# Kernel optimization log

Measured on AMD Instinct MI355X. Metric: run time of the kernel, lower is better.

Reference implementation:

```python
import jax, jax.numpy as jnp
import numpy as np

HEADS = 16
HEAD_DIM = 64
HIDDEN = HEADS * HEAD_DIM  # 1024
COMPRESSION = 1.0  # concat([o, p], -1) forces compressed seq len == T, i.e. scale 1
LN_EPS = 1e-5


def _interp_linear_seq(x, scale):
    # F.interpolate(mode='linear', align_corners=False) along the sequence axis.
    # x: [B, T, C] -> [B, int(T*scale), C]
    T = x.shape[1]
    S = int(T * scale)
    src = (jnp.arange(S, dtype=jnp.float32) + 0.5) / scale - 0.5
    src = jnp.clip(src, 0.0, T - 1)
    lo = jnp.floor(src).astype(jnp.int32)
    hi = jnp.minimum(lo + 1, T - 1)
    w = (src - lo.astype(jnp.float32))[None, :, None]
    return x[:, lo] * (1.0 - w) + x[:, hi] * w


def _rotary(x):
    # rotate-half rotary embedding; x: [B, S, h, d]
    S, d = x.shape[1], x.shape[3]
    inv_freq = 1.0 / (10000.0 ** (jnp.arange(0, d, 2, dtype=jnp.float32) / d))
    ang = jnp.arange(S, dtype=jnp.float32)[:, None] * inv_freq  # [S, d/2]
    cos = jnp.cos(ang)[None, :, None, :]
    sin = jnp.sin(ang)[None, :, None, :]
    x1, x2 = jnp.split(x, 2, axis=-1)
    return jnp.concatenate([x1 * cos - x2 * sin, x1 * sin + x2 * cos], axis=-1)


def setup_inputs() -> dict:
    key = jax.random.key(0)
    ks = jax.random.split(key, 4)
    B, T = 4, 2048
    x = jax.random.normal(ks[0], (B, T, HIDDEN), dtype=jnp.float32)
    ln_gamma = jnp.ones((HIDDEN,), dtype=jnp.float32)
    ln_beta = jnp.zeros((HIDDEN,), dtype=jnp.float32)
    w_in = jax.random.normal(ks[1], (HIDDEN, 7 * HIDDEN), dtype=jnp.float32) * (HIDDEN ** -0.5)
    w_out = jax.random.normal(ks[2], (5 * HIDDEN, HIDDEN), dtype=jnp.float32) * ((5 * HIDDEN) ** -0.5)
    b_out = jnp.zeros((HIDDEN,), dtype=jnp.float32)
    return {"x": x, "ln_gamma": ln_gamma, "ln_beta": ln_beta,
            "w_in": w_in, "w_out": w_out, "b_out": b_out}


def reference(x, ln_gamma, ln_beta, w_in, w_out, b_out):
    B, T, _ = x.shape
    # LayerNorm
    mu = jnp.mean(x, axis=-1, keepdims=True)
    var = jnp.mean(jnp.square(x - mu), axis=-1, keepdims=True)
    xn = (x - mu) / jnp.sqrt(var + LN_EPS) * ln_gamma + ln_beta
    # fused QKVP projection (no bias)
    qkvp = xn @ w_in  # [B, T, 7*HIDDEN]
    q, k, v, p = jnp.split(qkvp, [HIDDEN, 2 * HIDDEN, 3 * HIDDEN], axis=-1)
    # linear-interpolation compression of k, v, p along the sequence axis
    k = _interp_linear_seq(k, COMPRESSION)
    v = _interp_linear_seq(v, COMPRESSION)
    p = _interp_linear_seq(p, COMPRESSION)
    S = k.shape[1]
    q = q.reshape(B, T, HEADS, HEAD_DIM)
    k = k.reshape(B, S, HEADS, HEAD_DIM)
    v = v.reshape(B, S, HEADS, HEAD_DIM)
    q = _rotary(q)
    k = _rotary(k)
    # manual softmax attention (no mask in the original)
    a = jnp.einsum('bihd,bjhd->bhij', q, k) * (HEAD_DIM ** -0.5)
    a = jax.nn.softmax(a, axis=-1)
    o = jnp.einsum('bhij,bjhd->bihd', a, v).reshape(B, T, HIDDEN)
    # GELU side branch (torch F.gelu default = exact erf gelu)
    p = jax.nn.gelu(p, approximate=False)
    return jnp.concatenate([o, p], axis=-1) @ w_out + b_out
```

## Files before the change

### kernel.cpp

```cpp
#include <hip/hip_runtime.h>
#include <hip/hip_bf16.h>
#include <math.h>

typedef short bf16x8 __attribute__((ext_vector_type(8)));
typedef float f32x4 __attribute__((ext_vector_type(4)));
typedef float f32x16 __attribute__((ext_vector_type(16)));

#define HEADS 16
#define HDIM 64
#define HID 1024
#define B_ 4
#define T_ 2048
#define BT_ (B_*T_)
#define N1 (7*HID)
#define K2 (5*HID)

#define SM_SCALE_LOG2E 0.18033688011111793f

__device__ __forceinline__ float bf2f(unsigned short u) {
  union { unsigned int i; float f; } c; c.i = ((unsigned int)u) << 16; return c.f;
}
__device__ __forceinline__ unsigned short f2bf(float f) {
  __hip_bfloat16 h = __float2bfloat16(f);
  return __builtin_bit_cast(unsigned short, h);
}
__device__ __forceinline__ unsigned int cvt_pk_bf16(float a, float b) {
  unsigned int r;
  asm("v_cvt_pk_bf16_f32 %0, %1, %2" : "=v"(r) : "v"(a), "v"(b));
  return r;
}
__device__ __forceinline__ void permswap(unsigned int& d, unsigned int& s) {
  asm volatile("v_permlane32_swap_b32 %0, %1" : "+v"(d), "+v"(s));
}
__device__ __forceinline__ float gelu_fast(float x) {
  float y = 0.7978845608028654f * (x + 0.044715f * x * x * x);
  float e = exp2f(y * 2.8853900817779268f);
  float t = 1.f - 2.f / (e + 1.f);
  return 0.5f * x * (1.f + t);
}

__global__ __launch_bounds__(256) void tcast_kernel(const float* __restrict__ in,
                                                    unsigned short* __restrict__ out,
                                                    int R, int C) {
  __shared__ float tile[64][65];
  int tx = threadIdx.x & 63;
  int ty = threadIdx.x >> 6;
  long r0 = (long)blockIdx.y * 64;
  long c0 = (long)blockIdx.x * 64;
#pragma unroll
  for (int i = 0; i < 16; i++) {
    int r = ty + i * 4;
    tile[r][tx] = in[(r0 + r) * C + c0 + tx];
  }
  __syncthreads();
#pragma unroll
  for (int i = 0; i < 16; i++) {
    int rr = ty + i * 4;
    out[(c0 + rr) * R + r0 + tx] = f2bf(tile[tx][rr]);
  }
}

__global__ __launch_bounds__(256) void ln_kernel(const float* __restrict__ x,
                                                 const float* __restrict__ g,
                                                 const float* __restrict__ b,
                                                 unsigned short* __restrict__ xn) {
  int row = blockIdx.x, tid = threadIdx.x;
  float4 v = reinterpret_cast<const float4*>(x + (long)row * HID)[tid];
  float s = v.x + v.y + v.z + v.w;
  float sq = v.x * v.x + v.y * v.y + v.z * v.z + v.w * v.w;
#pragma unroll
  for (int off = 32; off > 0; off >>= 1) { s += __shfl_down(s, off); sq += __shfl_down(sq, off); }
  __shared__ float red[8];
  int wid = tid >> 6, lane = tid & 63;
  if (lane == 0) { red[wid] = s; red[4 + wid] = sq; }
  __syncthreads();
  if (tid == 0) {
    red[0] = red[0] + red[1] + red[2] + red[3];
    red[4] = red[4] + red[5] + red[6] + red[7];
  }
  __syncthreads();
  float mean = red[0] * (1.f / HID);
  float var  = red[4] * (1.f / HID) - mean * mean;
  float rstd = rsqrtf(var + 1e-5f);
  float4 gv = reinterpret_cast<const float4*>(g)[tid];
  float4 bv = reinterpret_cast<const float4*>(b)[tid];
  ushort4 o;
  o.x = f2bf((v.x - mean) * rstd * gv.x + bv.x);
  o.y = f2bf((v.y - mean) * rstd * gv.y + bv.y);
  o.z = f2bf((v.z - mean) * rstd * gv.z + bv.z);
  o.w = f2bf((v.w - mean) * rstd * gv.w + bv.w);
  reinterpret_cast<ushort4*>(xn + (long)row * HID)[tid] = o;
}

__device__ __forceinline__ void gemm_core_db(const unsigned short* __restrict__ A,
                                             const unsigned short* __restrict__ BT,
                                             unsigned short* As, unsigned short* Bs,
                                             int K, int lda, int ldb,
                                             long row0, long col0,
                                             int lane, int wid, f32x4 (&acc)[4][4]) {
  int l15 = lane & 15, lq = lane >> 4;
  int srow = lane >> 2;
  int schnk = lane & 3;
  int r0s = wid * 32 + srow;
  int r1s = r0s + 16;
  int slot0 = schnk ^ ((r0s >> 1) & 3);
  int slot1 = schnk ^ ((r1s >> 1) & 3);
  const unsigned short* a0 = A + (row0 + r0s) * (long)lda + schnk * 8;
  const unsigned short* a1 = A + (row0 + r1s) * (long)lda + schnk * 8;
  const unsigned short* b0 = BT + (col0 + r0s) * (long)ldb + schnk * 8;
  const unsigned short* b1 = BT + (col0 + r1s) * (long)ldb + schnk * 8;
  int wm = (wid & 1) * 64, wn = (wid >> 1) * 64;
  int NT = K / 32;

  bf16x8 ar0 = *reinterpret_cast<const bf16x8*>(a0);
  bf16x8 ar1 = *reinterpret_cast<const bf16x8*>(a1);
  bf16x8 br0 = *reinterpret_cast<const bf16x8*>(b0);
  bf16x8 br1 = *reinterpret_cast<const bf16x8*>(b1);
  *reinterpret_cast<bf16x8*>(&As[r0s * 32 + slot0 * 8]) = ar0;
  *reinterpret_cast<bf16x8*>(&As[r1s * 32 + slot1 * 8]) = ar1;
  *reinterpret_cast<bf16x8*>(&Bs[r0s * 32 + slot0 * 8]) = br0;
  *reinterpret_cast<bf16x8*>(&Bs[r1s * 32 + slot1 * 8]) = br1;
  ar0 = *reinterpret_cast<const bf16x8*>(a0 + 32);
  ar1 = *reinterpret_cast<const bf16x8*>(a1 + 32);
  br0 = *reinterpret_cast<const bf16x8*>(b0 + 32);
  br1 = *reinterpret_cast<const bf16x8*>(b1 + 32);
  __syncthreads();

  int cur = 0;
  for (int t = 0; t < NT; t++) {
    const unsigned short* Asr = As + cur * 4096;
    const unsigned short* Bsr = Bs + cur * 4096;
    bf16x8 af[4], bfv[4];
#pragma unroll
    for (int m = 0; m < 4; m++) {
      int r = wm + m * 16 + l15;
      af[m] = *reinterpret_cast<const bf16x8*>(&Asr[r * 32 + (lq ^ ((r >> 1) & 3)) * 8]);
    }
#pragma unroll
    for (int n = 0; n < 4; n++) {
      int r = wn + n * 16 + l15;
      bfv[n] = *reinterpret_cast<const bf16x8*>(&Bsr[r * 32 + (lq ^ ((r >> 1) & 3)) * 8]);
    }
    if (t + 1 < NT) {
      unsigned short* Asw = As + (cur ^ 1) * 4096;
      unsigned short* Bsw = Bs + (cur ^ 1) * 4096;
      *reinterpret_cast<bf16x8*>(&Asw[r0s * 32 + slot0 * 8]) = ar0;
      *reinterpret_cast<bf16x8*>(&Asw[r1s * 32 + slot1 * 8]) = ar1;
      *reinterpret_cast<bf16x8*>(&Bsw[r0s * 32 + slot0 * 8]) = br0;
      *reinterpret_cast<bf16x8*>(&Bsw[r1s * 32 + slot1 * 8]) = br1;
    }
    if (t + 2 < NT) {
      long ko = (long)(t + 2) * 32;
      ar0 = *reinterpret_cast<const bf16x8*>(a0 + ko);
      ar1 = *reinterpret_cast<const bf16x8*>(a1 + ko);
      br0 = *reinterpret_cast<const bf16x8*>(b0 + ko);
      br1 = *reinterpret_cast<const bf16x8*>(b1 + ko);
    }
#pragma unroll
    for (int m = 0; m < 4; m++)
#pragma unroll
      for (int n = 0; n < 4; n++)
        acc[m][n] = __builtin_amdgcn_mfma_f32_16x16x32_bf16(af[m], bfv[n], acc[m][n], 0, 0, 0);
    __syncthreads();
    cur ^= 1;
  }
}

__global__ __launch_bounds__(256) void gemm1_fused(const unsigned short* __restrict__ A,
                                                   const unsigned short* __restrict__ BT,
                                                   unsigned short* __restrict__ q_r,
                                                   unsigned short* __restrict__ k_r,
                                                   unsigned short* __restrict__ v_t,
                                                   unsigned short* __restrict__ C5) {
  __shared__ unsigned short smem[18432];
  unsigned short* As = smem;
  unsigned short* Bs = smem + 8192;
  int tid = threadIdx.x, lane = tid & 63, wid = tid >> 6;
  long row0 = (long)blockIdx.y * 128;
  long col0 = (long)blockIdx.x * 128;
  f32x4 acc[4][4] = {};
  gemm_core_db(A, BT, As, Bs, HID, HID, HID, row0, col0, lane, wid, acc);

  int wm = (wid & 1) * 64, wn = (wid >> 1) * 64;
  long row_base = row0 + wm;
  int b = (int)(row_base >> 11);
  int t_base = (int)(row_base & 2047);
  int col_base = (int)col0 + wn;
  int region = col_base >> 10;
  int l15 = lane & 15, lq = lane >> 4;

  if (region <= 1) {
    unsigned short* dst = (region == 0) ? q_r : k_r;
    float osc = (region == 0) ? SM_SCALE_LOG2E : 1.0f;
    int head = (col_base & 1023) >> 6;
    long obase = (long)(b * 16 + head) * T_ * 64;
    float fr[2];
    fr[0] = __expf(-(float)l15 * 0.28782313662425572f);
    fr[1] = __expf(-(float)(16 + l15) * 0.28782313662425572f);
#pragma unroll
    for (int m = 0; m < 4; m++) {
#pragma unroll
      for (int j = 0; j < 4; j++) {
        int t = t_base + m * 16 + lq * 4 + j;
#pragma unroll
        for (int n = 0; n < 2; n++) {
          float sn, cs;
          __sincosf((float)t * fr[n], &sn, &cs);
          float xl = acc[m][n][j], xh = acc[m][n + 2][j];
          int d = n * 16 + l15;
          dst[obase + (long)t * 64 + d]      = f2bf((xl * cs - xh * sn) * osc);
          dst[obase + (long)t * 64 + d + 32] = f2bf((xl * sn + xh * cs) * osc);
        }
      }
    }
  } else if (region == 2) {
    int head = (col_base & 1023) >> 6;
    unsigned short* vt = smem + wid * 4608;
#pragma unroll
    for (int m = 0; m < 4; m++)
#pragma unroll
      for (int n = 0; n < 4; n++)
#pragma unroll
        for (int j = 0; j < 4; j++)
          vt[(n * 16 + l15) * 72 + m * 16 + lq * 4 + j] = f2bf(acc[m][n][j]);
    long obase = (long)(b * 16 + head) * 64 * T_;
#pragma unroll
    for (int i = 0; i < 8; i++) {
      int d = i * 8 + (lane >> 3);
      int tl = (lane & 7) * 8;
      bf16x8 v = *reinterpret_cast<const bf16x8*>(&vt[d * 72 + tl]);
      *reinterpret_cast<bf16x8*>(v_t + obase + (long)d * T_ + t_base + tl) = v;
    }
  } else {
    int colp = col_base - 3 * HID;
#pragma unroll
    for (int m = 0; m < 4; m++) {
#pragma unroll
      for (int j = 0; j < 4; j++) {
        long row = row_base + m * 16 + lq * 4 + j;
#pragma unroll
        for (int n = 0; n < 4; n++)
          C5[row * K2 + HID + colp + n * 16 + l15] = f2bf(gelu_fast(acc[m][n][j]));
      }
    }
  }
}

__global__ __launch_bounds__(256) void gemm_bt(const unsigned short* __restrict__ A,
                                               const unsigned short* __restrict__ BT,
                                               float* __restrict__ Cout,
                                               const float* __restrict__ bias,
                                               int K, int lda, int ldb, int ldc) {
  __shared__ unsigned short smem2[16384];
  unsigned short* As = smem2;
  unsigned short* Bs = smem2 + 8192;
  int tid = threadIdx.x, lane = tid & 63, wid = tid >> 6;
  long row0 = (long)blockIdx.y * 128;
  long col0 = (long)blockIdx.x * 128;
  f32x4 acc[4][4] = {};
  gemm_core_db(A, BT, As, Bs, K, lda, ldb, row0, col0, lane, wid, acc);
  int wm = (wid & 1) * 64, wn = (wid >> 1) * 64;
#pragma unroll
  for (int m = 0; m < 4; m++) {
#pragma unroll
    for (int n = 0; n < 4; n++) {
      long r = row0 + wm + m * 16 + (lane >> 4) * 4;
      long c = col0 + wn + n * 16 + (lane & 15);
#pragma unroll
      for (int j = 0; j < 4; j++)
        Cout[(r + j) * (long)ldc + c] = acc[m][n][j] + bias[c];
    }
  }
}

__global__ __launch_bounds__(256) void attn_kernel(const unsigned short* __restrict__ q_r,
                                                   const unsigned short* __restrict__ k_r,
                                                   const unsigned short* __restrict__ v_t,
                                                   unsigned short* __restrict__ C5) {
  int bh = blockIdx.x;
  int qt = blockIdx.y;
  int b = bh >> 4, h = bh & 15;
  int tid = threadIdx.x, lane = tid & 63, wid = tid >> 6;
  int l31 = lane & 31, hi = lane >> 5;
  __shared__ unsigned short Ks[2][64 * 64];
  __shared__ unsigned short Vts[2][64 * 64];

  const unsigned short* qbase = q_r + ((long)bh * T_ + qt * 128 + wid * 32) * 64;
  bf16x8 qf[4];
#pragma unroll
  for (int kk = 0; kk < 4; kk++)
    qf[kk] = *reinterpret_cast<const bf16x8*>(qbase + l31 * 64 + kk * 16 + hi * 8);

  f32x16 o_acc[2] = {};
  float l_run = 0.f;

  const unsigned short* kbase = k_r + (long)bh * T_ * 64;
  const unsigned short* vbase = v_t + (long)bh * 64 * T_;
  int srow = lane >> 3;
  int schnk = lane & 7;
  int slot = schnk ^ srow;

  bf16x8 kreg[2], vreg[2];
#pragma unroll
  for (int i = 0; i < 2; i++) {
    int c = wid * 2 + i;
    kreg[i] = *reinterpret_cast<const bf16x8*>(kbase + c * 512 + lane * 8);
    vreg[i] = *reinterpret_cast<const bf16x8*>(vbase + (long)(c * 8 + srow) * T_ + schnk * 8);
  }
#pragma unroll
  for (int i = 0; i < 2; i++) {
    int r = (wid * 2 + i) * 8 + srow;
    *reinterpret_cast<bf16x8*>(&Ks[0][r * 64 + slot * 8])  = kreg[i];
    *reinterpret_cast<bf16x8*>(&Vts[0][r * 64 + slot * 8]) = vreg[i];
  }
#pragma unroll
  for (int i = 0; i < 2; i++) {
    int c = wid * 2 + i;
    kreg[i] = *reinterpret_cast<const bf16x8*>(kbase + 4096 + c * 512 + lane * 8);
    vreg[i] = *reinterpret_cast<const bf16x8*>(vbase + (long)(c * 8 + srow) * T_ + 64 + schnk * 8);
  }
  __syncthreads();

  int cur = 0;
  for (int kt = 0; kt < 32; kt++) {
    if (kt < 31) {
#pragma unroll
      for (int i = 0; i < 2; i++) {
        int r = (wid * 2 + i) * 8 + srow;
        *reinterpret_cast<bf16x8*>(&Ks[cur ^ 1][r * 64 + slot * 8])  = kreg[i];
        *reinterpret_cast<bf16x8*>(&Vts[cur ^ 1][r * 64 + slot * 8]) = vreg[i];
      }
    }
    if (kt < 30) {
#pragma unroll
      for (int i = 0; i < 2; i++) {
        int c = wid * 2 + i;
        kreg[i] = *reinterpret_cast<const bf16x8*>(kbase + (kt + 2) * 4096 + c * 512 + lane * 8);
        vreg[i] = *reinterpret_cast<const bf16x8*>(vbase + (long)(c * 8 + srow) * T_ + (kt + 2) * 64 + schnk * 8);
      }
    }
    const unsigned short* Kc = Ks[cur];
    const unsigned short* Vc = Vts[cur];

    bf16x8 pa[4];
#pragma unroll
    for (int t2 = 0; t2 < 2; t2++) {
      f32x16 s2 = {};
      int krow = t2 * 32 + l31;
      __builtin_amdgcn_s_setprio(1);
#pragma unroll
      for (int kk = 0; kk < 4; kk++) {
        int c = kk * 2 + hi;
        bf16x8 kf = *reinterpret_cast<const bf16x8*>(&Kc[krow * 64 + (c ^ (krow & 7)) * 8]);
        s2 = __builtin_amdgcn_mfma_f32_32x32x16_bf16(kf, qf[kk], s2, 0, 0, 0);
      }
      __builtin_amdgcn_s_setprio(0);
      float p[16];
#pragma unroll
      for (int r = 0; r < 16; r++) p[r] = exp2f(s2[r]);
#pragma unroll
      for (int r = 0; r < 16; r++) l_run += p[r];
      unsigned int g0 = cvt_pk_bf16(p[0],  p[1]);
      unsigned int g1 = cvt_pk_bf16(p[2],  p[3]);
      unsigned int g2 = cvt_pk_bf16(p[4],  p[5]);
      unsigned int g3 = cvt_pk_bf16(p[6],  p[7]);
      unsigned int g4 = cvt_pk_bf16(p[8],  p[9]);
      unsigned int g5 = cvt_pk_bf16(p[10], p[11]);
      unsigned int g6 = cvt_pk_bf16(p[12], p[13]);
      unsigned int g7 = cvt_pk_bf16(p[14], p[15]);
      permswap(g0, g2);
      permswap(g1, g3);
      permswap(g4, g6);
      permswap(g5, g7);
      uint4 u0; u0.x = g0; u0.y = g1; u0.z = g2; u0.w = g3;
      uint4 u1; u1.x = g4; u1.y = g5; u1.z = g6; u1.w = g7;
      pa[t2 * 2]     = __builtin_bit_cast(bf16x8, u0);
      pa[t2 * 2 + 1] = __builtin_bit_cast(bf16x8, u1);
    }
    __builtin_amdgcn_s_setprio(1);
#pragma unroll
    for (int dt = 0; dt < 2; dt++) {
      int vrow = dt * 32 + l31;
#pragma unroll
      for (int kc = 0; kc < 4; kc++) {
        int c = kc * 2 + hi;
        bf16x8 vf = *reinterpret_cast<const bf16x8*>(&Vc[vrow * 64 + (c ^ (vrow & 7)) * 8]);
        o_acc[dt] = __builtin_amdgcn_mfma_f32_32x32x16_bf16(pa[kc], vf, o_acc[dt], 0, 0, 0);
      }
    }
    __builtin_amdgcn_s_setprio(0);
    __syncthreads();
    cur ^= 1;
  }
  float l = l_run;
  l += __shfl_xor(l, 32);
#pragma unroll
  for (int r = 0; r < 16; r++) {
    int qr = (r & 3) + 8 * (r >> 2) + 4 * hi;
    float inv = 1.0f / __shfl(l, qr);
    int tl = qt * 128 + wid * 32 + qr;
    long row = (long)b * T_ + tl;
#pragma unroll
    for (int dt = 0; dt < 2; dt++) {
      int col = h * 64 + dt * 32 + l31;
      C5[row * K2 + col] = f2bf(o_acc[dt][r] * inv);
    }
  }
}

extern "C" void kernel_launch(void* const* d_in, const int* in_sizes, int n_in,
                              void* d_out, int out_size, void* d_ws, size_t ws_size,
                              hipStream_t stream) {
  const float* x     = (const float*)d_in[0];
  const float* g     = (const float*)d_in[1];
  const float* be    = (const float*)d_in[2];
  const float* w_in  = (const float*)d_in[3];
  const float* w_out = (const float*)d_in[4];
  const float* b_out = (const float*)d_in[5];
  float* out = (float*)d_out;

  char* ws = (char*)d_ws;
  size_t off = 0;
  auto alloc = [&](size_t bytes) {
    void* p = ws + off;
    off += (bytes + 255) & ~(size_t)255;
    return p;
  };
  unsigned short* xn     = (unsigned short*)alloc((size_t)BT_ * HID * 2);
  unsigned short* w_inT  = (unsigned short*)alloc((size_t)N1 * HID * 2);
  unsigned short* w_outT = (unsigned short*)alloc((size_t)HID * K2 * 2);
  unsigned short* q_rb   = (unsigned short*)alloc((size_t)BT_ * HID * 2);
  unsigned short* k_rb   = (unsigned short*)alloc((size_t)BT_ * HID * 2);
  unsigned short* v_tb   = (unsigned short*)alloc((size_t)BT_ * HID * 2);
  unsigned short* C5     = (unsigned short*)alloc((size_t)BT_ * K2 * 2);

  tcast_kernel<<<dim3(N1 / 64, HID / 64), 256, 0, stream>>>(w_in, w_inT, HID, N1);
  tcast_kernel<<<dim3(HID / 64, K2 / 64), 256, 0, stream>>>(w_out, w_outT, K2, HID);
  ln_kernel<<<BT_, 256, 0, stream>>>(x, g, be, xn);
  gemm1_fused<<<dim3(N1 / 128, BT_ / 128), 256, 0, stream>>>(xn, w_inT, q_rb, k_rb, v_tb, C5);
  attn_kernel<<<dim3(64, T_ / 128), 256, 0, stream>>>(q_rb, k_rb, v_tb, C5);
  gemm_bt<<<dim3(HID / 128, BT_ / 128), 256, 0, stream>>>(C5, w_outT, out, b_out,
                                                          K2, K2, K2, HID);
}
```

Baseline: 413.0 us.

## Enlarge QKVP GEMM tile to 256x128 with 8 waves and direct V^T stores

The fused input-projection GEMM now uses 256-row by 128-column tiles with 512 threads (8 waves in a 4x2 arrangement), so each B tile loaded into shared memory is reused across twice as many rows. This cuts global and LDS traffic per output. The V-transpose epilogue drops its shared-memory staging and writes packed 4-element bf16 chunks straight to global memory, giving up some store coalescing. The larger block doubles the LDS footprint and halves the grid, which may lower occupancy.

```diff
diff --git a/kernel.cpp b/kernel.cpp
--- a/kernel.cpp
+++ b/kernel.cpp
@@ -90,6 +90,138 @@
   o.z = f2bf((v.z - mean) * rstd * gv.z + bv.z);
   o.w = f2bf((v.w - mean) * rstd * gv.w + bv.w);
   reinterpret_cast<ushort4*>(xn + (long)row * HID)[tid] = o;
+}
+
+__global__ __launch_bounds__(512) void gemm1_fused(const unsigned short* __restrict__ A,
+                                                   const unsigned short* __restrict__ BT,
+                                                   unsigned short* __restrict__ q_r,
+                                                   unsigned short* __restrict__ k_r,
+                                                   unsigned short* __restrict__ v_t,
+                                                   unsigned short* __restrict__ C5) {
+  __shared__ unsigned short As[2 * 256 * 32];
+  __shared__ unsigned short Bs[2 * 128 * 32];
+  int tid = threadIdx.x, lane = tid & 63, wid = tid >> 6;
+  int l15 = lane & 15, lq = lane >> 4;
+  int wr = wid >> 1, wc = wid & 1;
+  long row0 = (long)blockIdx.y * 256;
+  long col0 = (long)blockIdx.x * 128;
+  f32x4 acc[4][4] = {};
+
+  int sr0 = tid >> 2;
+  int sr1 = sr0 + 128;
+  int sch = tid & 3;
+  int sl0 = sch ^ ((sr0 >> 1) & 3);
+  int sl1 = sch ^ ((sr1 >> 1) & 3);
+  const unsigned short* a0 = A + (row0 + sr0) * (long)HID + sch * 8;
+  const unsigned short* a1 = A + (row0 + sr1) * (long)HID + sch * 8;
+  const unsigned short* b0 = BT + (col0 + sr0) * (long)HID + sch * 8;
+
+  bf16x8 ar0 = *reinterpret_cast<const bf16x8*>(a0);
+  bf16x8 ar1 = *reinterpret_cast<const bf16x8*>(a1);
+  bf16x8 br0 = *reinterpret_cast<const bf16x8*>(b0);
+  *reinterpret_cast<bf16x8*>(&As[sr0 * 32 + sl0 * 8]) = ar0;
+  *reinterpret_cast<bf16x8*>(&As[sr1 * 32 + sl1 * 8]) = ar1;
+  *reinterpret_cast<bf16x8*>(&Bs[sr0 * 32 + sl0 * 8]) = br0;
+  ar0 = *reinterpret_cast<const bf16x8*>(a0 + 32);
+  ar1 = *reinterpret_cast<const bf16x8*>(a1 + 32);
+  br0 = *reinterpret_cast<const bf16x8*>(b0 + 32);
+  __syncthreads();
+
+  const int NT = HID / 32;
+  int cur = 0;
+  for (int t = 0; t < NT; t++) {
+    const unsigned short* Asr = As + cur * 8192;
+    const unsigned short* Bsr = Bs + cur * 4096;
+    bf16x8 af[4], bfv[4];
+#pragma unroll
+    for (int m = 0; m < 4; m++) {
+      int r = wr * 64 + m * 16 + l15;
+      af[m] = *reinterpret_cast<const bf16x8*>(&Asr[r * 32 + (lq ^ ((r >> 1) & 3)) * 8]);
+    }
+#pragma unroll
+    for (int n = 0; n < 4; n++) {
+      int r = wc * 64 + n * 16 + l15;
+      bfv[n] = *reinterpret_cast<const bf16x8*>(&Bsr[r * 32 + (lq ^ ((r >> 1) & 3)) * 8]);
+    }
+    if (t + 1 < NT) {
+      unsigned short* Asw = As + (cur ^ 1) * 8192;
+      unsigned short* Bsw = Bs + (cur ^ 1) * 4096;
+      *reinterpret_cast<bf16x8*>(&Asw[sr0 * 32 + sl0 * 8]) = ar0;
+      *reinterpret_cast<bf16x8*>(&Asw[sr1 * 32 + sl1 * 8]) = ar1;
+      *reinterpret_cast<bf16x8*>(&Bsw[sr0 * 32 + sl0 * 8]) = br0;
+    }
+    if (t + 2 < NT) {
+      long ko = (long)(t + 2) * 32;
+      ar0 = *reinterpret_cast<const bf16x8*>(a0 + ko);
+      ar1 = *reinterpret_cast<const bf16x8*>(a1 + ko);
+      br0 = *reinterpret_cast<const bf16x8*>(b0 + ko);
+    }
+#pragma unroll
+    for (int m = 0; m < 4; m++)
+#pragma unroll
+      for (int n = 0; n < 4; n++)
+        acc[m][n] = __builtin_amdgcn_mfma_f32_16x16x32_bf16(af[m], bfv[n], acc[m][n], 0, 0, 0);
+    __syncthreads();
+    cur ^= 1;
+  }
+
+  long row_base = row0 + wr * 64;
+  int b = (int)(row_base >> 11);
+  int t_base = (int)(row_base & 2047);
+  int col_base = (int)col0 + wc * 64;
+  int region = col_base >> 10;
+  int head = (col_base & 1023) >> 6;
+
+  if (region <= 1) {
+    unsigned short* dst = (region == 0) ? q_r : k_r;
+    float osc = (region == 0) ? SM_SCALE_LOG2E : 1.0f;
+    long obase = (long)(b * 16 + head) * T_ * 64;
+    float fr[2];
+    fr[0] = __expf(-(float)l15 * 0.28782313662425572f);
+    fr[1] = __expf(-(float)(16 + l15) * 0.28782313662425572f);
+#pragma unroll
+    for (int m = 0; m < 4; m++) {
+#pragma unroll
+      for (int j = 0; j < 4; j++) {
+        int t = t_base + m * 16 + lq * 4 + j;
+#pragma unroll
+        for (int n = 0; n < 2; n++) {
+          float sn, cs;
+          __sincosf((float)t * fr[n], &sn, &cs);
+          float xl = acc[m][n][j], xh = acc[m][n + 2][j];
+          int d = n * 16 + l15;
+          dst[obase + (long)t * 64 + d]      = f2bf((xl * cs - xh * sn) * osc);
+          dst[obase + (long)t * 64 + d + 32] = f2bf((xl * sn + xh * cs) * osc);
+        }
+      }
+    }
+  } else if (region == 2) {
+    long obase = (long)(b * 16 + head) * 64 * T_;
+#pragma unroll
+    for (int m = 0; m < 4; m++) {
+      int t0 = t_base + m * 16 + lq * 4;
+#pragma unroll
+      for (int n = 0; n < 4; n++) {
+        int d = n * 16 + l15;
+        uint2 w;
+        w.x = cvt_pk_bf16(acc[m][n][0], acc[m][n][1]);
+        w.y = cvt_pk_bf16(acc[m][n][2], acc[m][n][3]);
+        *reinterpret_cast<uint2*>(v_t + obase + (long)d * T_ + t0) = w;
+      }
+    }
+  } else {
+    int colp = col_base - 3 * HID;
+#pragma unroll
+    for (int m = 0; m < 4; m++) {
+#pragma unroll
+      for (int j = 0; j < 4; j++) {
+        long row = row_base + m * 16 + lq * 4 + j;
+#pragma unroll
+        for (int n = 0; n < 4; n++)
+          C5[row * K2 + HID + colp + n * 16 + l15] = f2bf(gelu_fast(acc[m][n][j]));
+      }
+    }
+  }
 }
 
 __device__ __forceinline__ void gemm_core_db(const unsigned short* __restrict__ A,
@@ -166,86 +298,6 @@
   }
 }
 
-__global__ __launch_bounds__(256) void gemm1_fused(const unsigned short* __restrict__ A,
-                                                   const unsigned short* __restrict__ BT,
-                                                   unsigned short* __restrict__ q_r,
-                                                   unsigned short* __restrict__ k_r,
-                                                   unsigned short* __restrict__ v_t,
-                                                   unsigned short* __restrict__ C5) {
-  __shared__ unsigned short smem[18432];
-  unsigned short* As = smem;
-  unsigned short* Bs = smem + 8192;
-  int tid = threadIdx.x, lane = tid & 63, wid = tid >> 6;
-  long row0 = (long)blockIdx.y * 128;
-  long col0 = (long)blockIdx.x * 128;
-  f32x4 acc[4][4] = {};
-  gemm_core_db(A, BT, As, Bs, HID, HID, HID, row0, col0, lane, wid, acc);
-
-  int wm = (wid & 1) * 64, wn = (wid >> 1) * 64;
-  long row_base = row0 + wm;
-  int b = (int)(row_base >> 11);
-  int t_base = (int)(row_base & 2047);
-  int col_base = (int)col0 + wn;
-  int region = col_base >> 10;
-  int l15 = lane & 15, lq = lane >> 4;
-
-  if (region <= 1) {
-    unsigned short* dst = (region == 0) ? q_r : k_r;
-    float osc = (region == 0) ? SM_SCALE_LOG2E : 1.0f;
-    int head = (col_base & 1023) >> 6;
-    long obase = (long)(b * 16 + head) * T_ * 64;
-    float fr[2];
-    fr[0] = __expf(-(float)l15 * 0.28782313662425572f);
-    fr[1] = __expf(-(float)(16 + l15) * 0.28782313662425572f);
-#pragma unroll
-    for (int m = 0; m < 4; m++) {
-#pragma unroll
-      for (int j = 0; j < 4; j++) {
-        int t = t_base + m * 16 + lq * 4 + j;
-#pragma unroll
-        for (int n = 0; n < 2; n++) {
-          float sn, cs;
-          __sincosf((float)t * fr[n], &sn, &cs);
-          float xl = acc[m][n][j], xh = acc[m][n + 2][j];
-          int d = n * 16 + l15;
-          dst[obase + (long)t * 64 + d]      = f2bf((xl * cs - xh * sn) * osc);
-          dst[obase + (long)t * 64 + d + 32] = f2bf((xl * sn + xh * cs) * osc);
-        }
-      }
-    }
-  } else if (region == 2) {
-    int head = (col_base & 1023) >> 6;
-    unsigned short* vt = smem + wid * 4608;
-#pragma unroll
-    for (int m = 0; m < 4; m++)
-#pragma unroll
-      for (int n = 0; n < 4; n++)
-#pragma unroll
-        for (int j = 0; j < 4; j++)
-          vt[(n * 16 + l15) * 72 + m * 16 + lq * 4 + j] = f2bf(acc[m][n][j]);
-    long obase = (long)(b * 16 + head) * 64 * T_;
-#pragma unroll
-    for (int i = 0; i < 8; i++) {
-      int d = i * 8 + (lane >> 3);
-      int tl = (lane & 7) * 8;
-      bf16x8 v = *reinterpret_cast<const bf16x8*>(&vt[d * 72 + tl]);
-      *reinterpret_cast<bf16x8*>(v_t + obase + (long)d * T_ + t_base + tl) = v;
-    }
-  } else {
-    int colp = col_base - 3 * HID;
-#pragma unroll
-    for (int m = 0; m < 4; m++) {
-#pragma unroll
-      for (int j = 0; j < 4; j++) {
-        long row = row_base + m * 16 + lq * 4 + j;
-#pragma unroll
-        for (int n = 0; n < 4; n++)
-          C5[row * K2 + HID + colp + n * 16 + l15] = f2bf(gelu_fast(acc[m][n][j]));
-      }
-    }
-  }
-}
-
 __global__ __launch_bounds__(256) void gemm_bt(const unsigned short* __restrict__ A,
                                                const unsigned short* __restrict__ BT,
                                                float* __restrict__ Cout,
@@ -437,7 +489,7 @@
   tcast_kernel<<<dim3(N1 / 64, HID / 64), 256, 0, stream>>>(w_in, w_inT, HID, N1);
   tcast_kernel<<<dim3(HID / 64, K2 / 64), 256, 0, stream>>>(w_out, w_outT, K2, HID);
   ln_kernel<<<BT_, 256, 0, stream>>>(x, g, be, xn);
-  gemm1_fused<<<dim3(N1 / 128, BT_ / 128), 256, 0, stream>>>(xn, w_inT, q_rb, k_rb, v_tb, C5);
+  gemm1_fused<<<dim3(N1 / 128, BT_ / 256), 512, 0, stream>>>(xn, w_inT, q_rb, k_rb, v_tb, C5);
   attn_kernel<<<dim3(64, T_ / 128), 256, 0, stream>>>(q_rb, k_rb, v_tb, C5);
   gemm_bt<<<dim3(HID / 128, BT_ / 128), 256, 0, stream>>>(C5, w_outT, out, b_out,
                                                           K2, K2, K2, HID);
```

New measurement: 406.9 us. About the same (-1.5%).

## Use async global-to-LDS loads with triple-buffered GEMM pipeline

Applied to the files above, without the earlier changes.

Replaces the register-staged double-buffered GEMM mainloop with direct global_load_lds async copies into a three-stage LDS ring. Loads for tile t+2 are issued before the MFMA work on tile t, and the loop syncs with explicit vmcnt waits and raw s_barrier instead of __syncthreads. Swizzling moves to the source address side so the LDS writes stay contiguous per lane. LDS use per block grows to 48KB, which may lower occupancy.

```diff
diff --git a/kernel.cpp b/kernel.cpp
--- a/kernel.cpp
+++ b/kernel.cpp
@@ -37,6 +37,12 @@
   float e = exp2f(y * 2.8853900817779268f);
   float t = 1.f - 2.f / (e + 1.f);
   return 0.5f * x * (1.f + t);
+}
+
+typedef __attribute__((address_space(1))) const unsigned int gu32;
+typedef __attribute__((address_space(3))) unsigned int lu32;
+__device__ __forceinline__ void async16(const void* g, void* l) {
+  __builtin_amdgcn_global_load_lds((gu32*)g, (lu32*)l, 16, 0, 0);
 }
 
 __global__ __launch_bounds__(256) void tcast_kernel(const float* __restrict__ in,
@@ -92,77 +98,72 @@
   reinterpret_cast<ushort4*>(xn + (long)row * HID)[tid] = o;
 }
 
-__device__ __forceinline__ void gemm_core_db(const unsigned short* __restrict__ A,
-                                             const unsigned short* __restrict__ BT,
-                                             unsigned short* As, unsigned short* Bs,
-                                             int K, int lda, int ldb,
-                                             long row0, long col0,
-                                             int lane, int wid, f32x4 (&acc)[4][4]) {
+__device__ __forceinline__ void gemm_core_t34(const unsigned short* __restrict__ A,
+                                              const unsigned short* __restrict__ BT,
+                                              unsigned short* As, unsigned short* Bs,
+                                              int K, int lda, int ldb,
+                                              long row0, long col0,
+                                              int lane, int wid, f32x4 (&acc)[4][4]) {
   int l15 = lane & 15, lq = lane >> 4;
-  int srow = lane >> 2;
-  int schnk = lane & 3;
-  int r0s = wid * 32 + srow;
-  int r1s = r0s + 16;
-  int slot0 = schnk ^ ((r0s >> 1) & 3);
-  int slot1 = schnk ^ ((r1s >> 1) & 3);
-  const unsigned short* a0 = A + (row0 + r0s) * (long)lda + schnk * 8;
-  const unsigned short* a1 = A + (row0 + r1s) * (long)lda + schnk * 8;
-  const unsigned short* b0 = BT + (col0 + r0s) * (long)ldb + schnk * 8;
-  const unsigned short* b1 = BT + (col0 + r1s) * (long)ldb + schnk * 8;
+  int d  = lane >> 2;
+  int ch = (lane & 3) ^ ((lane >> 3) & 3);
+  int R0 = wid * 32;
+  const unsigned short* aS0 = A + (row0 + R0 + d)      * (long)lda + ch * 8;
+  const unsigned short* aS1 = A + (row0 + R0 + 16 + d) * (long)lda + ch * 8;
+  const unsigned short* bS0 = BT + (col0 + R0 + d)      * (long)ldb + ch * 8;
+  const unsigned short* bS1 = BT + (col0 + R0 + 16 + d) * (long)ldb + ch * 8;
   int wm = (wid & 1) * 64, wn = (wid >> 1) * 64;
-  int NT = K / 32;
-
-  bf16x8 ar0 = *reinterpret_cast<const bf16x8*>(a0);
-  bf16x8 ar1 = *reinterpret_cast<const bf16x8*>(a1);
-  bf16x8 br0 = *reinterpret_cast<const bf16x8*>(b0);
-  bf16x8 br1 = *reinterpret_cast<const bf16x8*>(b1);
-  *reinterpret_cast<bf16x8*>(&As[r0s * 32 + slot0 * 8]) = ar0;
-  *reinterpret_cast<bf16x8*>(&As[r1s * 32 + slot1 * 8]) = ar1;
-  *reinterpret_cast<bf16x8*>(&Bs[r0s * 32 + slot0 * 8]) = br0;
-  *reinterpret_cast<bf16x8*>(&Bs[r1s * 32 + slot1 * 8]) = br1;
-  ar0 = *reinterpret_cast<const bf16x8*>(a0 + 32);
-  ar1 = *reinterpret_cast<const bf16x8*>(a1 + 32);
-  br0 = *reinterpret_cast<const bf16x8*>(b0 + 32);
-  br1 = *reinterpret_cast<const bf16x8*>(b1 + 32);
-  __syncthreads();
-
-  int cur = 0;
+  const int NT = K / 32;
+
+  unsigned short* A0 = As;         unsigned short* B0 = Bs;
+  unsigned short* A1 = As + 4096;  unsigned short* B1 = Bs + 4096;
+  unsigned short* A2 = As + 8192;  unsigned short* B2 = Bs + 8192;
+
+  async16(aS0, &A0[R0 * 32]);
+  async16(aS1, &A0[(R0 + 16) * 32]);
+  async16(bS0, &B0[R0 * 32]);
+  async16(bS1, &B0[(R0 + 16) * 32]);
+  async16(aS0 + 32, &A1[R0 * 32]);
+  async16(aS1 + 32, &A1[(R0 + 16) * 32]);
+  async16(bS0 + 32, &B1[R0 * 32]);
+  async16(bS1 + 32, &B1[(R0 + 16) * 32]);
+  asm volatile("s_waitcnt vmcnt(4)" ::: "memory");
+  __builtin_amdgcn_s_barrier();
+  __builtin_amdgcn_sched_barrier(0);
+
   for (int t = 0; t < NT; t++) {
-    const unsigned short* Asr = As + cur * 4096;
-    const unsigned short* Bsr = Bs + cur * 4096;
+    if (t + 2 < NT) {
+      long ko = (long)(t + 2) * 32;
+      async16(aS0 + ko, &A2[R0 * 32]);
+      async16(aS1 + ko, &A2[(R0 + 16) * 32]);
+      async16(bS0 + ko, &B2[R0 * 32]);
+      async16(bS1 + ko, &B2[(R0 + 16) * 32]);
+    }
     bf16x8 af[4], bfv[4];
 #pragma unroll
     for (int m = 0; m < 4; m++) {
       int r = wm + m * 16 + l15;
-      af[m] = *reinterpret_cast<const bf16x8*>(&Asr[r * 32 + (lq ^ ((r >> 1) & 3)) * 8]);
+      af[m] = *reinterpret_cast<const bf16x8*>(&A0[r * 32 + (lq ^ ((r >> 1) & 3)) * 8]);
     }
 #pragma unroll
     for (int n = 0; n < 4; n++) {
       int r = wn + n * 16 + l15;
-      bfv[n] = *reinterpret_cast<const bf16x8*>(&Bsr[r * 32 + (lq ^ ((r >> 1) & 3)) * 8]);
-    }
-    if (t + 1 < NT) {
-      unsigned short* Asw = As + (cur ^ 1) * 4096;
-      unsigned short* Bsw = Bs + (cur ^ 1) * 4096;
-      *reinterpret_cast<bf16x8*>(&Asw[r0s * 32 + slot0 * 8]) = ar0;
-      *reinterpret_cast<bf16x8*>(&Asw[r1s * 32 + slot1 * 8]) = ar1;
-      *reinterpret_cast<bf16x8*>(&Bsw[r0s * 32 + slot0 * 8]) = br0;
-      *reinterpret_cast<bf16x8*>(&Bsw[r1s * 32 + slot1 * 8]) = br1;
-    }
-    if (t + 2 < NT) {
-      long ko = (long)(t + 2) * 32;
-      ar0 = *reinterpret_cast<const bf16x8*>(a0 + ko);
-      ar1 = *reinterpret_cast<const bf16x8*>(a1 + ko);
-      br0 = *reinterpret_cast<const bf16x8*>(b0 + ko);
-      br1 = *reinterpret_cast<const bf16x8*>(b1 + ko);
+      bfv[n] = *reinterpret_cast<const bf16x8*>(&B0[r * 32 + (lq ^ ((r >> 1) & 3)) * 8]);
     }
 #pragma unroll
     for (int m = 0; m < 4; m++)
 #pragma unroll
       for (int n = 0; n < 4; n++)
         acc[m][n] = __builtin_amdgcn_mfma_f32_16x16x32_bf16(af[m], bfv[n], acc[m][n], 0, 0, 0);
-    __syncthreads();
-    cur ^= 1;
+    if (t + 2 < NT) {
+      asm volatile("s_waitcnt vmcnt(4) lgkmcnt(0)" ::: "memory");
+    } else {
+      asm volatile("s_waitcnt vmcnt(0) lgkmcnt(0)" ::: "memory");
+    }
+    __builtin_amdgcn_s_barrier();
+    __builtin_amdgcn_sched_barrier(0);
+    unsigned short* ta = A0; A0 = A1; A1 = A2; A2 = ta;
+    unsigned short* tb = B0; B0 = B1; B1 = B2; B2 = tb;
   }
 }
 
@@ -172,14 +173,14 @@
                                                    unsigned short* __restrict__ k_r,
                                                    unsigned short* __restrict__ v_t,
                                                    unsigned short* __restrict__ C5) {
-  __shared__ unsigned short smem[18432];
+  __shared__ unsigned short smem[24576];
   unsigned short* As = smem;
-  unsigned short* Bs = smem + 8192;
+  unsigned short* Bs = smem + 12288;
   int tid = threadIdx.x, lane = tid & 63, wid = tid >> 6;
   long row0 = (long)blockIdx.y * 128;
   long col0 = (long)blockIdx.x * 128;
   f32x4 acc[4][4] = {};
-  gemm_core_db(A, BT, As, Bs, HID, HID, HID, row0, col0, lane, wid, acc);
+  gemm_core_t34(A, BT, As, Bs, HID, HID, HID, row0, col0, lane, wid, acc);
 
   int wm = (wid & 1) * 64, wn = (wid >> 1) * 64;
   long row_base = row0 + wm;
@@ -207,9 +208,9 @@
           float sn, cs;
           __sincosf((float)t * fr[n], &sn, &cs);
           float xl = acc[m][n][j], xh = acc[m][n + 2][j];
-          int d = n * 16 + l15;
-          dst[obase + (long)t * 64 + d]      = f2bf((xl * cs - xh * sn) * osc);
-          dst[obase + (long)t * 64 + d + 32] = f2bf((xl * sn + xh * cs) * osc);
+          int dd = n * 16 + l15;
+          dst[obase + (long)t * 64 + dd]      = f2bf((xl * cs - xh * sn) * osc);
+          dst[obase + (long)t * 64 + dd + 32] = f2bf((xl * sn + xh * cs) * osc);
         }
       }
     }
@@ -226,10 +227,10 @@
     long obase = (long)(b * 16 + head) * 64 * T_;
 #pragma unroll
     for (int i = 0; i < 8; i++) {
-      int d = i * 8 + (lane >> 3);
+      int dd = i * 8 + (lane >> 3);
       int tl = (lane & 7) * 8;
-      bf16x8 v = *reinterpret_cast<const bf16x8*>(&vt[d * 72 + tl]);
-      *reinterpret_cast<bf16x8*>(v_t + obase + (long)d * T_ + t_base + tl) = v;
+      bf16x8 v = *reinterpret_cast<const bf16x8*>(&vt[dd * 72 + tl]);
+      *reinterpret_cast<bf16x8*>(v_t + obase + (long)dd * T_ + t_base + tl) = v;
     }
   } else {
     int colp = col_base - 3 * HID;
@@ -251,14 +252,14 @@
                                                float* __restrict__ Cout,
                                                const float* __restrict__ bias,
                                                int K, int lda, int ldb, int ldc) {
-  __shared__ unsigned short smem2[16384];
+  __shared__ unsigned short smem2[24576];
   unsigned short* As = smem2;
-  unsigned short* Bs = smem2 + 8192;
+  unsigned short* Bs = smem2 + 12288;
   int tid = threadIdx.x, lane = tid & 63, wid = tid >> 6;
   long row0 = (long)blockIdx.y * 128;
   long col0 = (long)blockIdx.x * 128;
   f32x4 acc[4][4] = {};
-  gemm_core_db(A, BT, As, Bs, K, lda, ldb, row0, col0, lane, wid, acc);
+  gemm_core_t34(A, BT, As, Bs, K, lda, ldb, row0, col0, lane, wid, acc);
   int wm = (wid & 1) * 64, wn = (wid >> 1) * 64;
 #pragma unroll
   for (int m = 0; m < 4; m++) {
```

Result: faster. 404.0 us (-2.2%).
